# Optimization experiments

Hardware: AMD Instinct MI355X
Metric: run time of the kernel (lower is better)

The kernel has to match this reference:

```python
import jax, jax.numpy as jnp
import numpy as np

EPS = 1e-6


def _mp_match(reps, att, kernel):
    """BiMPM multi-perspective match.
    reps: (B,L,D); att: (B,L,D) or (B,1,D); kernel: (M,D).
    Returns (B,L,1+M): [tanh(sum(reps*att)), tanh(sum_d reps*kernel_m*att)].
    """
    prod = reps * att                                   # (B,L,D)
    cos = jnp.tanh(jnp.sum(prod, axis=-1, keepdims=True))   # (B,L,1)
    mp = jnp.tanh(jnp.einsum('bld,md->blm', prod, kernel))  # (B,L,M)
    return jnp.concatenate([cos, mp], axis=-1)


def setup_inputs() -> dict:
    key = jax.random.key(0)
    ks = jax.random.split(key, 12)
    B, Llt, Lrt, D, M, A = 32, 128, 128, 512, 64, 128
    H = D // 2
    u = lambda k, shape: jax.random.uniform(k, shape, jnp.float32, -0.05, 0.05)  # keras 'uniform' init
    return {
        'reps_lt': jax.random.normal(ks[0], (B, Llt, D), jnp.float32),
        'h_lt_fw': jax.random.normal(ks[1], (B, H), jnp.float32),
        'h_lt_bw': jax.random.normal(ks[2], (B, H), jnp.float32),
        'reps_rt': jax.random.normal(ks[3], (B, Lrt, D), jnp.float32),
        'h_rt_fw': jax.random.normal(ks[4], (B, H), jnp.float32),
        'h_rt_bw': jax.random.normal(ks[5], (B, H), jnp.float32),
        'kernel_full': u(ks[6], (M, D)),
        'kernel_mpool': u(ks[7], (M, D)),
        'attn_w1': u(ks[8], (D, A)),
        'diag_w': u(ks[9], (A,)),
        'kernel_att': u(ks[10], (M, D)),
        'kernel_maxatt': u(ks[11], (M, D)),
    }


def reference(reps_lt, h_lt_fw, h_lt_bw, reps_rt, h_rt_fw, h_rt_bw,
              kernel_full, kernel_mpool, attn_w1, diag_w,
              kernel_att, kernel_maxatt):
    # ---- full match: each left timestep vs last BiLSTM state of right ----
    h_rt = jnp.concatenate([h_rt_fw, h_rt_bw], axis=-1)[:, None, :]  # (B,1,D)
    full = _mp_match(reps_lt, h_rt, kernel_full)                     # (B,Ll,1+M)

    # ---- max-pooling match ----
    # t[b,r,l,m] = tanh(sum_d R[b,r,d]*K[m,d]*L[b,l,d]); max over right positions r
    r_scaled = jnp.einsum('brd,md->brmd', reps_rt, kernel_mpool)     # (B,Lr,M,D)
    t = jnp.tanh(jnp.einsum('brmd,bld->brlm', r_scaled, reps_lt))    # (B,Lr,Ll,M)
    mpool = jnp.max(t, axis=1)                                       # (B,Ll,M)

    # ---- attentive match ----
    a_lt = jnp.tanh(reps_lt @ attn_w1) * diag_w                      # (B,Ll,A)
    a_rt = jnp.tanh(reps_rt @ attn_w1)                               # (B,Lr,A)
    scores = jnp.einsum('bla,bra->blr', a_lt, a_rt)                  # (B,Ll,Lr)
    probs = jax.nn.softmax(scores, axis=-1)
    att = jnp.einsum('blr,brd->bld', probs, reps_rt)                 # (B,Ll,D)
    attentive = _mp_match(reps_lt, att, kernel_att)                  # (B,Ll,1+M)

    # ---- max-attentive match ----
    num = jnp.einsum('bld,brd->blr', reps_lt, reps_rt)
    n_lt = jnp.sqrt(jnp.maximum(jnp.sum(reps_lt * reps_lt, -1), EPS))[:, :, None]
    n_rt = jnp.sqrt(jnp.maximum(jnp.sum(reps_rt * reps_rt, -1), EPS))[:, None, :]
    rel = num / n_rt / n_lt                                          # (B,Ll,Lr)
    idx = jnp.argmax(rel, axis=2)                                    # (B,Ll) int
    max_att = jnp.take_along_axis(reps_rt, idx[:, :, None], axis=1)  # (B,Ll,D)
    maxatt = _mp_match(reps_lt, max_att, kernel_maxatt)              # (B,Ll,1+M)

    return jnp.concatenate([full, mpool, attentive, maxatt], axis=-1)  # (B,Ll,3+4M)
```

## Files before the change

kernel.cpp:

```cpp
#include <hip/hip_runtime.h>
#include <hip/hip_bf16.h>
#include <math.h>
#include <stdint.h>

typedef __attribute__((ext_vector_type(8))) short short8;
typedef __attribute__((ext_vector_type(4))) float float4v;

#define DEV static __device__ __forceinline__

DEV float bflo(unsigned int u) { union { unsigned int i; float f; } v; v.i = u << 16; return v.f; }
DEV float bfhi(unsigned int u) { union { unsigned int i; float f; } v; v.i = u & 0xffff0000u; return v.f; }
DEV unsigned short f2bf(float f) {
    union { float f; unsigned int i; } v; v.f = f;
    unsigned int x = v.i;
    return (unsigned short)((x + 0x7fffu + ((x >> 16) & 1u)) >> 16);
}
DEV unsigned int pack2(float a, float b) { return (unsigned int)f2bf(a) | ((unsigned int)f2bf(b) << 16); }
#if __has_builtin(__builtin_amdgcn_cvt_pk_bf16_f32)
DEV unsigned int pack2_fast(float a, float b) {
    typedef __attribute__((ext_vector_type(2))) short short2v;
    short2v r = __builtin_amdgcn_cvt_pk_bf16_f32(a, b);
    union { short2v s; unsigned int u; } v; v.s = r; return v.u;
}
#else
DEV unsigned int pack2_fast(float a, float b) { return pack2(a, b); }
#endif
DEV void unpack8(uint4 u, float* f) {
    f[0]=bflo(u.x); f[1]=bfhi(u.x); f[2]=bflo(u.y); f[3]=bfhi(u.y);
    f[4]=bflo(u.z); f[5]=bfhi(u.z); f[6]=bflo(u.w); f[7]=bfhi(u.w);
}

DEV void async16(const unsigned short* g, unsigned short* l) {
    __builtin_amdgcn_global_load_lds(
        (const __attribute__((address_space(1))) unsigned int*)g,
        (__attribute__((address_space(3))) unsigned int*)l, 16, 0, 0);
}

__global__ __launch_bounds__(256) void prep_kernel(const float* __restrict__ lt,
                                                   const float* __restrict__ rt,
                                                   const float* __restrict__ kf,
                                                   const float* __restrict__ kmp,
                                                   const float* __restrict__ ka,
                                                   const float* __restrict__ km,
                                                   const float* __restrict__ w1,
                                                   unsigned short* __restrict__ ltb,
                                                   unsigned short* __restrict__ rtb,
                                                   unsigned short* __restrict__ kb,
                                                   unsigned short* __restrict__ w1t,
                                                   unsigned short* __restrict__ rtbT,
                                                   double* __restrict__ rsq) {
    __shared__ double ws2[2][2];
    __shared__ float tile[32][33];
    int bid = blockIdx.x, t = threadIdx.x;
    if (bid < 1024) {
        bool isRt = bid >= 512;
        int base = (isRt ? (bid - 512) : bid) * 8;
        int rl = t >> 7;
        int c  = t & 127;
        const float* srcb = isRt ? rt : lt;
        unsigned short* dstb = isRt ? rtb : ltb;
        #pragma unroll
        for (int p = 0; p < 4; ++p) {
            int row = base + p * 2 + rl;
            const float* src = srcb + (size_t)row * 512;
            float4 v = *(const float4*)(src + c * 4);
            ushort4 o;
            o.x = f2bf(v.x); o.y = f2bf(v.y); o.z = f2bf(v.z); o.w = f2bf(v.w);
            *(ushort4*)(dstb + (size_t)row * 512 + c * 4) = o;
            if (isRt) {
                double s = (double)v.x * v.x + (double)v.y * v.y
                         + (double)v.z * v.z + (double)v.w * v.w;
                #pragma unroll
                for (int off = 1; off < 64; off <<= 1) s += __shfl_xor(s, off, 64);
                if ((c & 63) == 0) ws2[rl][c >> 6] = s;
                __syncthreads();
                if (c == 0) rsq[row] = 1.0 / sqrt(ws2[rl][0] + ws2[rl][1]);
                __syncthreads();
            }
        }
    } else if (bid < 1152) {
        int kbk = bid - 1024;
        int ksel = kbk >> 5;
        const float* src = (ksel == 0) ? kf : (ksel == 1) ? kmp : (ksel == 2) ? ka : km;
        int off = (kbk & 31) * 1024 + t * 4;
        float4 v = *(const float4*)(src + off);
        ushort4 o;
        o.x = f2bf(v.x); o.y = f2bf(v.y); o.z = f2bf(v.z); o.w = f2bf(v.w);
        *(ushort4*)(kb + ksel * 32768 + off) = o;
    } else if (bid < 1216) {
        int b2 = bid - 1152;
        int d0 = (b2 & 15) * 32, a0 = (b2 >> 4) * 32;
        int r = t >> 5, c = t & 31;
        #pragma unroll
        for (int i = 0; i < 32; i += 8)
            tile[r + i][c] = w1[(size_t)(d0 + r + i) * 128 + a0 + c];
        __syncthreads();
        #pragma unroll
        for (int i = 0; i < 32; i += 8)
            w1t[(size_t)(a0 + r + i) * 512 + d0 + c] = f2bf(tile[c][r + i]);
    } else {
        int b3 = bid - 1216;
        int b = b3 >> 6;
        int tid = b3 & 63;
        int d0 = (tid & 15) * 32;
        int r0 = (tid >> 4) * 32;
        int r = t >> 5, c = t & 31;
        #pragma unroll
        for (int i = 0; i < 32; i += 8)
            tile[r + i][c] = rt[(size_t)(b * 128 + r0 + r + i) * 512 + d0 + c];
        __syncthreads();
        #pragma unroll
        for (int i = 0; i < 32; i += 8)
            rtbT[(size_t)(b * 512 + d0 + r + i) * 128 + r0 + c] = f2bf(tile[c][r + i]);
    }
}

__global__ __launch_bounds__(256, 3) void uber_kernel(
        const unsigned short* __restrict__ ltb,
        const unsigned short* __restrict__ rtb,
        const unsigned short* __restrict__ kmb,
        const unsigned short* __restrict__ w1t,
        const float* __restrict__ diag,
        unsigned short* __restrict__ a_all,
        const float* __restrict__ ltf,
        const float* __restrict__ rtf,
        const double* __restrict__ rsq,
        int* __restrict__ idxout,
        float* __restrict__ out) {
    __shared__ __align__(16) unsigned char smem[52224];
    int bx = blockIdx.x;
    int t = threadIdx.x;
    int wave = t >> 6, lane = t & 63;
    int q = lane >> 4, col = lane & 15, kq = q * 8;

    if (bx < 2048) {
        int xcd = bx & 7, jj = bx >> 3;
        int b = xcd * 4 + (jj >> 6);
        int m = jj & 63;
        unsigned short* ltS = (unsigned short*)smem;
        unsigned short* rtL = (unsigned short*)(smem + 16384);
        float (*mx)[2] = (float(*)[2])(smem + 16384 + 32768);
        int wl = wave & 1, wr = wave >> 1;
        const unsigned short* ltp = ltb + (size_t)b * 65536;
        const unsigned short* rtp = rtb + (size_t)b * 65536;
        const unsigned short* kr = kmb + (size_t)m * 512;
        int srow = t >> 3, cg8 = t & 7, cg = cg8 * 8;
        int gsw = (cg8 ^ (srow & 7)) * 8;
        int wbase = (t & ~63) * 8;

        #pragma unroll
        for (int it = 0; it < 4; ++it)
            async16(rtp + (size_t)(it * 32 + srow) * 512 + gsw,
                    rtL + it * 2048 + wbase);
        uint4 pk = *(const uint4*)(kr + cg);
        uint4 plt[4];
        #pragma unroll
        for (int it = 0; it < 4; ++it)
            plt[it] = *(const uint4*)(ltp + (size_t)(it * 32 + srow) * 512 + cg);

        float4v acc[4][4] = {};
        for (int k0i = 0; k0i < 8; ++k0i) {
            float kf8[8]; unpack8(pk, kf8);
            #pragma unroll
            for (int it = 0; it < 4; ++it) {
                int row = it * 32 + srow;
                float lf[8]; unpack8(plt[it], lf);
                uint4 s;
                s.x = pack2_fast(lf[0] * kf8[0], lf[1] * kf8[1]);
                s.y = pack2_fast(lf[2] * kf8[2], lf[3] * kf8[3]);
                s.z = pack2_fast(lf[4] * kf8[4], lf[5] * kf8[5]);
                s.w = pack2_fast(lf[6] * kf8[6], lf[7] * kf8[7]);
                *(uint4*)&ltS[row * 64 + gsw] = s;
            }
            __syncthreads();
            if (k0i < 7) {
                int k0n = (k0i + 1) * 64;
                int bofs = ((k0i + 1) & 1) * 8192;
                #pragma unroll
                for (int it = 0; it < 4; ++it)
                    async16(rtp + (size_t)(it * 32 + srow) * 512 + k0n + gsw,
                            rtL + bofs + it * 2048 + wbase);
                pk = *(const uint4*)(kr + k0n + cg);
                #pragma unroll
                for (int it = 0; it < 4; ++it)
                    plt[it] = *(const uint4*)(ltp + (size_t)(it * 32 + srow) * 512 + k0n + cg);
            }
            const unsigned short* rb = rtL + (k0i & 1) * 8192;
            #pragma unroll
            for (int kk = 0; kk < 64; kk += 32) {
                short8 af[4], bfr[4];
                #pragma unroll
                for (int i = 0; i < 4; ++i) {
                    int rowA = wl * 64 + i * 16 + col;
                    int slotA = ((kk >> 3) + q) ^ (rowA & 7);
                    af[i] = *(const short8*)&ltS[rowA * 64 + slotA * 8];
                }
                #pragma unroll
                for (int j = 0; j < 4; ++j) {
                    int row = wr * 64 + j * 16 + col;
                    int slot = ((kk >> 3) + q) ^ (row & 7);
                    bfr[j] = *(const short8*)&rb[row * 64 + slot * 8];
                }
                #pragma unroll
                for (int i = 0; i < 4; ++i)
                    #pragma unroll
                    for (int j = 0; j < 4; ++j)
                        acc[i][j] = __builtin_amdgcn_mfma_f32_16x16x32_bf16(af[i], bfr[j], acc[i][j], 0, 0, 0);
            }
            __syncthreads();
        }
        #pragma unroll
        for (int i = 0; i < 4; ++i)
            #pragma unroll
            for (int ii = 0; ii < 4; ++ii) {
                float v = fmaxf(fmaxf(acc[i][0][ii], acc[i][1][ii]), fmaxf(acc[i][2][ii], acc[i][3][ii]));
                #pragma unroll
                for (int off = 1; off < 16; off <<= 1) v = fmaxf(v, __shfl_xor(v, off, 64));
                if (col == 0) mx[wl * 64 + i * 16 + q * 4 + ii][wr] = v;
            }
        __syncthreads();
        if (t < 128)
            out[((size_t)(b * 128 + t)) * 259 + 65 + m] = tanhf(fmaxf(mx[t][0], mx[t][1]));

    } else if (bx < 2560) {
        int idA = bx - 2048;
        int xcd = idA & 7, jj = idA >> 3;
        int b = xcd * 4 + (jj >> 4);
        int L0 = (jj & 15) * 8;
        float* ltS = (float*)smem;
        float* buf = (float*)(smem + 16384);
        double* dvs = (double*)(smem + 49152);
        float* wv1 = (float*)(smem + 49152 + 128);
        float* wv2 = wv1 + 16;
        int* wi1 = (int*)(wv2 + 16);
        int* wi2 = wi1 + 16;
        int* candi = wi2 + 16;
        {
            int row = t >> 5, c0 = (t & 31) * 16;
            const float* src = ltf + ((size_t)(b * 128 + L0 + row)) * 512 + c0;
            #pragma unroll
            for (int i = 0; i < 4; ++i)
                *(float4*)&ltS[row * 512 + c0 + i * 4] = *(const float4*)(src + i * 4);
        }
        int lg = t >> 7;
        int rg = (t >> 2) & 31;
        int ds = t & 3;
        float acc[4][4] = {{0.f}};
        for (int p = 0; p < 8; ++p) {
            __syncthreads();
            {
                int row = t >> 1, c0 = (t & 1) * 32;
                const float* src = rtf + ((size_t)(b * 128 + row)) * 512 + p * 64 + c0;
                float f[32];
                #pragma unroll
                for (int i = 0; i < 8; ++i)
                    *(float4*)&f[i * 4] = *(const float4*)(src + i * 4);
                int base = row * 64;
                #pragma unroll
                for (int gg = 0; gg < 4; ++gg) {
                    int g = (t & 1) * 4 + gg;
                    int o = ((g ^ (row & 7)) * 8);
                    #pragma unroll
                    for (int k = 0; k < 8; ++k) buf[base + o + k] = f[gg * 8 + k];
                }
            }
            __syncthreads();
            #pragma unroll
            for (int sub = 0; sub < 2; ++sub) {
                int dloc = ds * 16 + sub * 8;
                int dglob = p * 64 + dloc;
                float a[4][8];
                #pragma unroll
                for (int i = 0; i < 4; ++i)
                    #pragma unroll
                    for (int k = 0; k < 8; ++k) a[i][k] = ltS[(lg * 4 + i) * 512 + dglob + k];
                int g = dloc >> 3;
                #pragma unroll
                for (int j = 0; j < 4; ++j) {
                    int r = rg + j * 32;
                    const float* rp = &buf[r * 64 + ((g ^ (r & 7)) * 8)];
                    float rv[8];
                    #pragma unroll
                    for (int k = 0; k < 8; ++k) rv[k] = rp[k];
                    #pragma unroll
                    for (int i = 0; i < 4; ++i)
                        #pragma unroll
                        for (int k = 0; k < 8; ++k)
                            acc[i][j] = fmaf(a[i][k], rv[k], acc[i][j]);
                }
            }
        }
        #pragma unroll
        for (int i = 0; i < 4; ++i)
            #pragma unroll
            for (int j = 0; j < 4; ++j) {
                acc[i][j] += __shfl_xor(acc[i][j], 1, 64);
                acc[i][j] += __shfl_xor(acc[i][j], 2, 64);
            }
        float v1[4], v2[4]; int i1[4], i2[4];
        #pragma unroll
        for (int i = 0; i < 4; ++i) {
            v1[i] = -3.0e38f; v2[i] = -3.0e38f; i1[i] = 0; i2[i] = 1;
            #pragma unroll
            for (int j = 0; j < 4; ++j) {
                int r = rg + j * 32;
                float s = acc[i][j] * (float)rsq[b * 128 + r];
                if (s > v1[i]) { v2[i] = v1[i]; i2[i] = i1[i]; v1[i] = s; i1[i] = r; }
                else if (s > v2[i]) { v2[i] = s; i2[i] = r; }
            }
        }
        #pragma unroll
        for (int off = 4; off < 64; off <<= 1) {
            #pragma unroll
            for (int i = 0; i < 4; ++i) {
                float u1 = __shfl_xor(v1[i], off, 64); int j1 = __shfl_xor(i1[i], off, 64);
                float u2 = __shfl_xor(v2[i], off, 64); int j2 = __shfl_xor(i2[i], off, 64);
                if (u1 > v1[i]) {
                    float ov = v1[i]; int oi = i1[i];
                    v1[i] = u1; i1[i] = j1;
                    if (u2 > ov) { v2[i] = u2; i2[i] = j2; } else { v2[i] = ov; i2[i] = oi; }
                } else if (u1 > v2[i]) { v2[i] = u1; i2[i] = j1; }
            }
        }
        if (lane == 0) {
            #pragma unroll
            for (int i = 0; i < 4; ++i) {
                int l = lg * 4 + i, h = wave & 1;
                wv1[l * 2 + h] = v1[i]; wi1[l * 2 + h] = i1[i];
                wv2[l * 2 + h] = v2[i]; wi2[l * 2 + h] = i2[i];
            }
        }
        __syncthreads();
        if (t < 8) {
            float a1 = wv1[t * 2], a2 = wv2[t * 2]; int ai1 = wi1[t * 2], ai2 = wi2[t * 2];
            float b1 = wv1[t * 2 + 1], b2 = wv2[t * 2 + 1]; int bi1 = wi1[t * 2 + 1], bi2 = wi2[t * 2 + 1];
            int ri1, ri2;
            if (b1 > a1) {
                ri1 = bi1;
                if (b2 > a1) { ri2 = bi2; } else { ri2 = ai1; }
            } else {
                ri1 = ai1;
                if (b1 > a2) { ri2 = bi1; } else { ri2 = ai2; }
            }
            candi[t * 2] = ri1; candi[t * 2 + 1] = ri2;
            (void)a2; (void)b2; (void)ai2; (void)bi2;
        }
        __syncthreads();
        {
            int dotid = t >> 4;
            int sub = t & 15;
            int l = dotid >> 1, c = dotid & 1;
            int r = candi[l * 2 + c];
            const float* lrow = ltf + ((size_t)(b * 128 + L0 + l)) * 512;
            const float* rrow = rtf + ((size_t)(b * 128 + r)) * 512;
            double s = 0.0;
            #pragma unroll 8
            for (int k = 0; k < 32; ++k) {
                int d = sub * 32 + k;
                s = fma((double)lrow[d], (double)rrow[d], s);
            }
            #pragma unroll
            for (int off = 1; off < 16; off <<= 1) s += __shfl_xor(s, off, 64);
            if (sub == 0) dvs[l * 2 + c] = s * rsq[b * 128 + r];
        }
        __syncthreads();
        if (t < 8) {
            int ia = candi[t * 2], ib = candi[t * 2 + 1];
            double va = dvs[t * 2], vb = dvs[t * 2 + 1];
            int res = (vb > va || (vb == va && ib < ia)) ? ib : ia;
            idxout[b * 128 + L0 + t] = res;
        }

    } else {
        int R0 = (bx - 2560) * 32;
        unsigned short (*aS)[72] = (unsigned short(*)[72])smem;
        unsigned short (*bS)[72] = (unsigned short(*)[72])(smem + 4608);
        float* diagS = (float*)(smem + 4608 + 18432);
        int wl = wave & 1, wr = wave >> 1;
        if (t < 128) diagS[t] = diag[t];
        const unsigned short* src = (R0 < 4096) ? (ltb + (size_t)R0 * 512) : (rtb + (size_t)(R0 - 4096) * 512);
        float4v acc[4] = {};
        for (int k0 = 0; k0 < 512; k0 += 64) {
            {
                int row = t >> 3, cg = (t & 7) * 8;
                *(uint4*)&aS[row][cg] = *(const uint4*)(src + (size_t)row * 512 + k0 + cg);
            }
            #pragma unroll
            for (int it = 0; it < 4; ++it) {
                int id = it * 256 + t;
                int row = id >> 3, cg = (id & 7) * 8;
                *(uint4*)&bS[row][cg] = *(const uint4*)(w1t + (size_t)row * 512 + k0 + cg);
            }
            __syncthreads();
            #pragma unroll
            for (int kk = 0; kk < 64; kk += 32) {
                short8 af = *(const short8*)&aS[wl * 16 + col][kk + kq];
                #pragma unroll
                for (int j = 0; j < 4; ++j) {
                    short8 bf = *(const short8*)&bS[wr * 64 + j * 16 + col][kk + kq];
                    acc[j] = __builtin_amdgcn_mfma_f32_16x16x32_bf16(af, bf, acc[j], 0, 0, 0);
                }
            }
            __syncthreads();
        }
        bool isLt = (R0 < 4096);
        #pragma unroll
        for (int j = 0; j < 4; ++j)
            #pragma unroll
            for (int ii = 0; ii < 4; ++ii) {
                int rowl = wl * 16 + q * 4 + ii;
                int n = wr * 64 + j * 16 + col;
                float v = tanhf(acc[j][ii]);
                if (isLt) v *= diagS[n];
                a_all[((size_t)(R0 + rowl)) * 128 + n] = f2bf(v);
            }
    }
}

__global__ __launch_bounds__(512, 4) void tail_kernel(
        const unsigned short* __restrict__ a_all,
        const unsigned short* __restrict__ rtb,
        const unsigned short* __restrict__ rtbT,
        const float* __restrict__ ltf,
        const unsigned short* __restrict__ kb,
        const float* __restrict__ hfw,
        const float* __restrict__ hbw,
        const int* __restrict__ idxp,
        float* __restrict__ out) {
    __shared__ __align__(16) unsigned char smem[81664];
    int bx = blockIdx.x;
    int t = threadIdx.x;
    int wave = t >> 6, lane = t & 63;
    int q = lane >> 4, col = lane & 15, kq = q * 8;

    if (bx < 256) {
        int b = bx & 31, lg = bx >> 5;
        int L0 = lg * 16;
        unsigned short (*altS)[136]  = (unsigned short(*)[136])(smem);
        unsigned short (*artS)[136]  = (unsigned short(*)[136])(smem + 4352);
        unsigned short (*prodsF)[520]= (unsigned short(*)[520])(smem + 55552);
        float (*pmax)[8] = (float(*)[8])(smem + 80640);
        float (*psum)[8] = (float(*)[8])(smem + 81152);
        const unsigned short* kb_att = kb + 2 * 32768;

        if (t < 256) {
            int row = t >> 4, c0 = (t & 15) * 8;
            *(uint4*)&altS[row][c0] = *(const uint4*)(a_all + ((size_t)(b * 128 + L0 + row)) * 128 + c0);
        }
        {
            int row = t >> 2, c0 = (t & 3) * 32;
            const unsigned short* src = a_all + ((size_t)(4096 + b * 128 + row)) * 128 + c0;
            #pragma unroll
            for (int i = 0; i < 4; ++i)
                *(uint4*)&artS[row][c0 + i * 8] = *(const uint4*)(src + i * 8);
        }
        __syncthreads();

        float4v acc = {};
        #pragma unroll
        for (int kk = 0; kk < 128; kk += 32) {
            short8 af = *(const short8*)&altS[col][kk + kq];
            short8 bf = *(const short8*)&artS[wave * 16 + col][kk + kq];
            acc = __builtin_amdgcn_mfma_f32_16x16x32_bf16(af, bf, acc, 0, 0, 0);
        }
        float m4[4], p4[4];
        #pragma unroll
        for (int ii = 0; ii < 4; ++ii) {
            float v = acc[ii];
            #pragma unroll
            for (int off = 1; off < 16; off <<= 1) v = fmaxf(v, __shfl_xor(v, off, 64));
            m4[ii] = v;
        }
        if (col == 0) {
            #pragma unroll
            for (int ii = 0; ii < 4; ++ii) pmax[q * 4 + ii][wave] = m4[ii];
        }
        __syncthreads();
        #pragma unroll
        for (int ii = 0; ii < 4; ++ii) {
            float M = pmax[q * 4 + ii][0];
            #pragma unroll
            for (int w = 1; w < 8; ++w) M = fmaxf(M, pmax[q * 4 + ii][w]);
            p4[ii] = expf(acc[ii] - M);
            float s = p4[ii];
            #pragma unroll
            for (int off = 1; off < 16; off <<= 1) s += __shfl_xor(s, off, 64);
            m4[ii] = s;
        }
        if (col == 0) {
            #pragma unroll
            for (int ii = 0; ii < 4; ++ii) psum[q * 4 + ii][wave] = m4[ii];
        }
        __syncthreads();
        unsigned short* Pb = (unsigned short*)smem;
        #pragma unroll
        for (int ii = 0; ii < 4; ++ii) {
            float S = psum[q * 4 + ii][0] + psum[q * 4 + ii][1] + psum[q * 4 + ii][2] + psum[q * 4 + ii][3]
                    + psum[q * 4 + ii][4] + psum[q * 4 + ii][5] + psum[q * 4 + ii][6] + psum[q * 4 + ii][7];
            Pb[(q * 4 + ii) * 136 + wave * 16 + col] = f2bf(p4[ii] / S);
        }

        unsigned short* Bc = (unsigned short*)(smem + 4352);
        float* attF = (float*)(smem + 39168);
        const unsigned short* rtT = rtbT + (size_t)b * 65536;
        for (int cc = 0; cc < 4; ++cc) {
            #pragma unroll
            for (int i = 0; i < 4; ++i) {
                int rid = i * 32 + (t >> 4);
                int d   = (rid >> 4) * 64 + cc * 16 + (rid & 15);
                int sg  = (t & 15) ^ (rid & 15);
                async16(rtT + (size_t)d * 128 + sg * 8, Bc + i * 4096 + t * 8);
            }
            __syncthreads();
            float4v pacc = {};
            #pragma unroll
            for (int ks = 0; ks < 4; ++ks) {
                short8 afP = *(const short8*)&Pb[col * 136 + ks * 32 + kq];
                short8 bfB = *(const short8*)&Bc[(wave * 16 + col) * 128 + (((ks * 4 + q) ^ col) * 8)];
                pacc = __builtin_amdgcn_mfma_f32_16x16x32_bf16(afP, bfB, pacc, 0, 0, 0);
            }
            #pragma unroll
            for (int ii = 0; ii < 4; ++ii)
                attF[(q * 4 + ii) * 512 + wave * 64 + cc * 16 + col] = pacc[ii];
            __syncthreads();
        }

        int l = t >> 5, cd = t & 31;
        float a8[2][8];
        #pragma unroll
        for (int pass = 0; pass < 2; ++pass) {
            *(float4*)&a8[pass][0] = *(const float4*)&attF[l * 512 + pass * 256 + cd * 8];
            *(float4*)&a8[pass][4] = *(const float4*)&attF[l * 512 + pass * 256 + cd * 8 + 4];
        }
        __syncthreads();

        int grow = b * 128 + L0 + l;
        const float* ltrow = ltf + (size_t)grow * 512;
        float csum = 0.f;
        #pragma unroll
        for (int pass = 0; pass < 2; ++pass) {
            int d0 = pass * 256 + cd * 8;
            float lf[8];
            *(float4*)&lf[0] = *(const float4*)(ltrow + d0);
            *(float4*)&lf[4] = *(const float4*)(ltrow + d0 + 4);
            float pf[8];
            #pragma unroll
            for (int k = 0; k < 8; ++k) { pf[k] = lf[k] * a8[pass][k]; csum += pf[k]; }
            uint4 o;
            o.x = pack2(pf[0], pf[1]); o.y = pack2(pf[2], pf[3]);
            o.z = pack2(pf[4], pf[5]); o.w = pack2(pf[6], pf[7]);
            *(uint4*)&prodsF[l][d0] = o;
        }
        #pragma unroll
        for (int off = 1; off < 32; off <<= 1) csum += __shfl_xor(csum, off, 64);
        if (cd == 0) out[(size_t)grow * 259 + 129] = tanhf(csum);

        unsigned short* Ks = &artS[0][0];
        float* red = (float*)(smem + 39168);
        for (int half = 0; half < 2; ++half) {
            __syncthreads();
            {
                int row = t >> 4, c0 = (t & 15) * 32;
                const unsigned short* src = kb_att + ((size_t)(half * 32 + row)) * 512 + c0;
                #pragma unroll
                for (int i = 0; i < 4; ++i)
                    *(uint4*)&Ks[row * 520 + c0 + i * 8] = *(const uint4*)(src + i * 8);
            }
            __syncthreads();
            float4v pacc[2] = {};
            #pragma unroll
            for (int kk = 0; kk < 64; kk += 32) {
                short8 af = *(const short8*)&prodsF[col][wave * 64 + kk + kq];
                #pragma unroll
                for (int j = 0; j < 2; ++j) {
                    short8 bf = *(const short8*)&Ks[(j * 16 + col) * 520 + wave * 64 + kk + kq];
                    pacc[j] = __builtin_amdgcn_mfma_f32_16x16x32_bf16(af, bf, pacc[j], 0, 0, 0);
                }
            }
            #pragma unroll
            for (int j = 0; j < 2; ++j)
                #pragma unroll
                for (int ii = 0; ii < 4; ++ii)
                    red[((wave * 2 + j) * 16 + q * 4 + ii) * 16 + col] = pacc[j][ii];
            __syncthreads();
            {
                int ll = t >> 5, jm = t & 31;
                int j = jm >> 4, mc = jm & 15;
                float s = 0.f;
                #pragma unroll
                for (int w = 0; w < 8; ++w) s += red[((w * 2 + j) * 16 + ll) * 16 + mc];
                out[((size_t)(b * 128 + L0 + ll)) * 259 + 130 + half * 32 + jm] = tanhf(s);
            }
        }

    } else {
        int idB = bx - 256;
        int lg = idB & 7, b = (idB >> 3) & 31;
        int mode = (idB >> 8) ? 2 : 0;
        int L0 = lg * 16;
        unsigned short (*prods)[520] = (unsigned short(*)[520])smem;
        unsigned short* Ks = (unsigned short*)(smem + 16640);
        float* red = (float*)(smem + 49920);
        const unsigned short* Kp = kb + (size_t)((mode == 0) ? 0 : 3 * 32768);
        int obase = (mode == 0) ? 0 : 194;

        if (t < 256) {
            int l = t >> 4, c = t & 15;
            int grow = b * 128 + L0 + l;
            const float* ltrow = ltf + (size_t)grow * 512;
            const unsigned short* avrow = 0;
            if (mode == 2) avrow = rtb + ((size_t)(b * 128 + idxp[grow])) * 512;
            float csum = 0.f;
            #pragma unroll
            for (int pass = 0; pass < 4; ++pass) {
                int d0 = pass * 128 + c * 8;
                float lf[8], af[8], pf[8];
                *(float4*)&lf[0] = *(const float4*)(ltrow + d0);
                *(float4*)&lf[4] = *(const float4*)(ltrow + d0 + 4);
                if (mode == 0) {
                    const float* h = (d0 < 256) ? (hfw + b * 256 + d0) : (hbw + b * 256 + d0 - 256);
                    *(float4*)&af[0] = *(const float4*)h;
                    *(float4*)&af[4] = *(const float4*)(h + 4);
                } else {
                    uint4 av = *(const uint4*)(avrow + d0);
                    unpack8(av, af);
                }
                #pragma unroll
                for (int k = 0; k < 8; ++k) { pf[k] = lf[k] * af[k]; csum += pf[k]; }
                uint4 o;
                o.x = pack2(pf[0], pf[1]); o.y = pack2(pf[2], pf[3]);
                o.z = pack2(pf[4], pf[5]); o.w = pack2(pf[6], pf[7]);
                *(uint4*)&prods[l][d0] = o;
            }
            #pragma unroll
            for (int off = 1; off < 16; off <<= 1) csum += __shfl_xor(csum, off, 64);
            if (c == 0) out[(size_t)grow * 259 + obase] = tanhf(csum);
        }
        for (int half = 0; half < 2; ++half) {
            {
                int row = t >> 4, c0 = (t & 15) * 32;
                const unsigned short* src = Kp + ((size_t)(half * 32 + row)) * 512 + c0;
                #pragma unroll
                for (int i = 0; i < 4; ++i)
                    *(uint4*)&Ks[row * 520 + c0 + i * 8] = *(const uint4*)(src + i * 8);
            }
            __syncthreads();
            float4v acc2[2] = {};
            #pragma unroll
            for (int kk = 0; kk < 64; kk += 32) {
                short8 af = *(const short8*)&prods[col][wave * 64 + kk + kq];
                #pragma unroll
                for (int j = 0; j < 2; ++j) {
                    short8 bf = *(const short8*)&Ks[(j * 16 + col) * 520 + wave * 64 + kk + kq];
                    acc2[j] = __builtin_amdgcn_mfma_f32_16x16x32_bf16(af, bf, acc2[j], 0, 0, 0);
                }
            }
            #pragma unroll
            for (int j = 0; j < 2; ++j)
                #pragma unroll
                for (int ii = 0; ii < 4; ++ii)
                    red[((wave * 2 + j) * 16 + q * 4 + ii) * 16 + col] = acc2[j][ii];
            __syncthreads();
            {
                int ll = t >> 5, jm = t & 31;
                int j = jm >> 4, mc = jm & 15;
                float s = 0.f;
                #pragma unroll
                for (int w = 0; w < 8; ++w) s += red[((w * 2 + j) * 16 + ll) * 16 + mc];
                out[((size_t)(b * 128 + L0 + ll)) * 259 + obase + 1 + half * 32 + jm] = tanhf(s);
            }
            __syncthreads();
        }
    }
}

extern "C" void kernel_launch(void* const* d_in, const int* in_sizes, int n_in,
                              void* d_out, int out_size, void* d_ws, size_t ws_size,
                              hipStream_t stream) {
    const float* lt  = (const float*)d_in[0];
    const float* rt  = (const float*)d_in[3];
    const float* hfw = (const float*)d_in[4];
    const float* hbw = (const float*)d_in[5];
    const float* kf  = (const float*)d_in[6];
    const float* kmp = (const float*)d_in[7];
    const float* w1  = (const float*)d_in[8];
    const float* dia = (const float*)d_in[9];
    const float* ka  = (const float*)d_in[10];
    const float* km  = (const float*)d_in[11];
    float* out = (float*)d_out;

    char* wsb = (char*)d_ws;
    unsigned short* ltb16 = (unsigned short*)(wsb);
    unsigned short* rtb16 = (unsigned short*)(wsb + 4194304);
    unsigned short* kb16  = (unsigned short*)(wsb + 8388608);
    unsigned short* w1t   = (unsigned short*)(wsb + 8650752);
    unsigned short* a_all = (unsigned short*)(wsb + 8781824);
    unsigned short* rtbT  = (unsigned short*)(wsb + 10878976);
    double*         rsq   = (double*)(wsb + 15073280);
    int*            idx   = (int*)(wsb + 15106048);

    prep_kernel<<<3264, 256, 0, stream>>>(lt, rt, kf, kmp, ka, km, w1, ltb16, rtb16, kb16, w1t, rtbT, rsq);
    uber_kernel<<<2816, 256, 0, stream>>>(ltb16, rtb16, kb16 + 32768, w1t, dia, a_all,
                                          lt, rt, rsq, idx, out);
    tail_kernel<<<768, 512, 0, stream>>>(a_all, rtb16, rtbT, lt, kb16, hfw, hbw, idx, out);
}
```

Baseline: 174.4 us.

## Move max-pooling GEMM blocks into tail kernel, interleaved with attentive/match blocks

Moves the max-pooling match blocks out of the middle kernel into the final kernel. They now run as 512-thread blocks with 8 waves, each wave holding a narrower 4x2 accumulator tile. Blocks are interleaved in groups of 11 (8 mpool, 1 attentive, 2 mp-match), so the independent mpool work can overlap with the dependent attentive and max-attentive work. The middle kernel shrinks to the argmax and attention-projection blocks. The trade-off is fewer accumulators per wave and a heavier last kernel.

```diff
diff --git a/kernel.cpp b/kernel.cpp
--- a/kernel.cpp
+++ b/kernel.cpp
@@ -115,115 +115,24 @@
     }
 }
 
-__global__ __launch_bounds__(256, 3) void uber_kernel(
+__global__ __launch_bounds__(256, 3) void mid_kernel(
         const unsigned short* __restrict__ ltb,
         const unsigned short* __restrict__ rtb,
-        const unsigned short* __restrict__ kmb,
         const unsigned short* __restrict__ w1t,
         const float* __restrict__ diag,
         unsigned short* __restrict__ a_all,
         const float* __restrict__ ltf,
         const float* __restrict__ rtf,
         const double* __restrict__ rsq,
-        int* __restrict__ idxout,
-        float* __restrict__ out) {
+        int* __restrict__ idxout) {
     __shared__ __align__(16) unsigned char smem[52224];
     int bx = blockIdx.x;
     int t = threadIdx.x;
     int wave = t >> 6, lane = t & 63;
     int q = lane >> 4, col = lane & 15, kq = q * 8;
 
-    if (bx < 2048) {
-        int xcd = bx & 7, jj = bx >> 3;
-        int b = xcd * 4 + (jj >> 6);
-        int m = jj & 63;
-        unsigned short* ltS = (unsigned short*)smem;
-        unsigned short* rtL = (unsigned short*)(smem + 16384);
-        float (*mx)[2] = (float(*)[2])(smem + 16384 + 32768);
-        int wl = wave & 1, wr = wave >> 1;
-        const unsigned short* ltp = ltb + (size_t)b * 65536;
-        const unsigned short* rtp = rtb + (size_t)b * 65536;
-        const unsigned short* kr = kmb + (size_t)m * 512;
-        int srow = t >> 3, cg8 = t & 7, cg = cg8 * 8;
-        int gsw = (cg8 ^ (srow & 7)) * 8;
-        int wbase = (t & ~63) * 8;
-
-        #pragma unroll
-        for (int it = 0; it < 4; ++it)
-            async16(rtp + (size_t)(it * 32 + srow) * 512 + gsw,
-                    rtL + it * 2048 + wbase);
-        uint4 pk = *(const uint4*)(kr + cg);
-        uint4 plt[4];
-        #pragma unroll
-        for (int it = 0; it < 4; ++it)
-            plt[it] = *(const uint4*)(ltp + (size_t)(it * 32 + srow) * 512 + cg);
-
-        float4v acc[4][4] = {};
-        for (int k0i = 0; k0i < 8; ++k0i) {
-            float kf8[8]; unpack8(pk, kf8);
-            #pragma unroll
-            for (int it = 0; it < 4; ++it) {
-                int row = it * 32 + srow;
-                float lf[8]; unpack8(plt[it], lf);
-                uint4 s;
-                s.x = pack2_fast(lf[0] * kf8[0], lf[1] * kf8[1]);
-                s.y = pack2_fast(lf[2] * kf8[2], lf[3] * kf8[3]);
-                s.z = pack2_fast(lf[4] * kf8[4], lf[5] * kf8[5]);
-                s.w = pack2_fast(lf[6] * kf8[6], lf[7] * kf8[7]);
-                *(uint4*)&ltS[row * 64 + gsw] = s;
-            }
-            __syncthreads();
-            if (k0i < 7) {
-                int k0n = (k0i + 1) * 64;
-                int bofs = ((k0i + 1) & 1) * 8192;
-                #pragma unroll
-                for (int it = 0; it < 4; ++it)
-                    async16(rtp + (size_t)(it * 32 + srow) * 512 + k0n + gsw,
-                            rtL + bofs + it * 2048 + wbase);
-                pk = *(const uint4*)(kr + k0n + cg);
-                #pragma unroll
-                for (int it = 0; it < 4; ++it)
-                    plt[it] = *(const uint4*)(ltp + (size_t)(it * 32 + srow) * 512 + k0n + cg);
-            }
-            const unsigned short* rb = rtL + (k0i & 1) * 8192;
-            #pragma unroll
-            for (int kk = 0; kk < 64; kk += 32) {
-                short8 af[4], bfr[4];
-                #pragma unroll
-                for (int i = 0; i < 4; ++i) {
-                    int rowA = wl * 64 + i * 16 + col;
-                    int slotA = ((kk >> 3) + q) ^ (rowA & 7);
-                    af[i] = *(const short8*)&ltS[rowA * 64 + slotA * 8];
-                }
-                #pragma unroll
-                for (int j = 0; j < 4; ++j) {
-                    int row = wr * 64 + j * 16 + col;
-                    int slot = ((kk >> 3) + q) ^ (row & 7);
-                    bfr[j] = *(const short8*)&rb[row * 64 + slot * 8];
-                }
-                #pragma unroll
-                for (int i = 0; i < 4; ++i)
-                    #pragma unroll
-                    for (int j = 0; j < 4; ++j)
-                        acc[i][j] = __builtin_amdgcn_mfma_f32_16x16x32_bf16(af[i], bfr[j], acc[i][j], 0, 0, 0);
-            }
-            __syncthreads();
-        }
-        #pragma unroll
-        for (int i = 0; i < 4; ++i)
-            #pragma unroll
-            for (int ii = 0; ii < 4; ++ii) {
-                float v = fmaxf(fmaxf(acc[i][0][ii], acc[i][1][ii]), fmaxf(acc[i][2][ii], acc[i][3][ii]));
-                #pragma unroll
-                for (int off = 1; off < 16; off <<= 1) v = fmaxf(v, __shfl_xor(v, off, 64));
-                if (col == 0) mx[wl * 64 + i * 16 + q * 4 + ii][wr] = v;
-            }
-        __syncthreads();
-        if (t < 128)
-            out[((size_t)(b * 128 + t)) * 259 + 65 + m] = tanhf(fmaxf(mx[t][0], mx[t][1]));
-
-    } else if (bx < 2560) {
-        int idA = bx - 2048;
+    if (bx < 512) {
+        int idA = bx;
         int xcd = idA & 7, jj = idA >> 3;
         int b = xcd * 4 + (jj >> 4);
         int L0 = (jj & 15) * 8;
@@ -372,7 +281,7 @@
         }
 
     } else {
-        int R0 = (bx - 2560) * 32;
+        int R0 = (bx - 512) * 32;
         unsigned short (*aS)[72] = (unsigned short(*)[72])smem;
         unsigned short (*bS)[72] = (unsigned short(*)[72])(smem + 4608);
         float* diagS = (float*)(smem + 4608 + 18432);
@@ -417,9 +326,11 @@
     }
 }
 
-__global__ __launch_bounds__(512, 4) void tail_kernel(
+__global__ __launch_bounds__(512, 4) void main_kernel(
+        const unsigned short* __restrict__ ltb,
+        const unsigned short* __restrict__ rtb,
+        const unsigned short* __restrict__ kmb,
         const unsigned short* __restrict__ a_all,
-        const unsigned short* __restrict__ rtb,
         const unsigned short* __restrict__ rtbT,
         const float* __restrict__ ltf,
         const unsigned short* __restrict__ kb,
@@ -433,8 +344,103 @@
     int wave = t >> 6, lane = t & 63;
     int q = lane >> 4, col = lane & 15, kq = q * 8;
 
-    if (bx < 256) {
-        int b = bx & 31, lg = bx >> 5;
+    int bxg = bx / 11;
+    int r11 = bx - bxg * 11;
+
+    if (r11 < 8) {
+        int mp = bxg * 8 + r11;
+        int xcd = mp & 7, jj = mp >> 3;
+        int b = xcd * 4 + (jj >> 6);
+        int m = jj & 63;
+        unsigned short* ltS = (unsigned short*)smem;
+        unsigned short* rtL = (unsigned short*)(smem + 16384);
+        float (*mx)[4] = (float(*)[4])(smem + 49152);
+        int wl = wave & 1, wr = wave >> 1;
+        const unsigned short* ltp = ltb + (size_t)b * 65536;
+        const unsigned short* rtp = rtb + (size_t)b * 65536;
+        const unsigned short* kr = kmb + (size_t)m * 512;
+        int srow = t >> 3, cg8 = t & 7, cg = cg8 * 8;
+        int gsw = (cg8 ^ (srow & 7)) * 8;
+
+        #pragma unroll
+        for (int it = 0; it < 2; ++it)
+            async16(rtp + (size_t)(it * 64 + srow) * 512 + gsw,
+                    rtL + it * 4096 + t * 8);
+        uint4 pk = *(const uint4*)(kr + cg);
+        uint4 plt[2];
+        #pragma unroll
+        for (int it = 0; it < 2; ++it)
+            plt[it] = *(const uint4*)(ltp + (size_t)(it * 64 + srow) * 512 + cg);
+
+        float4v acc[4][2] = {};
+        for (int k0i = 0; k0i < 8; ++k0i) {
+            float kf8[8]; unpack8(pk, kf8);
+            #pragma unroll
+            for (int it = 0; it < 2; ++it) {
+                int row = it * 64 + srow;
+                float lf[8]; unpack8(plt[it], lf);
+                uint4 s;
+                s.x = pack2_fast(lf[0] * kf8[0], lf[1] * kf8[1]);
+                s.y = pack2_fast(lf[2] * kf8[2], lf[3] * kf8[3]);
+                s.z = pack2_fast(lf[4] * kf8[4], lf[5] * kf8[5]);
+                s.w = pack2_fast(lf[6] * kf8[6], lf[7] * kf8[7]);
+                *(uint4*)&ltS[row * 64 + gsw] = s;
+            }
+            __syncthreads();
+            if (k0i < 7) {
+                int k0n = (k0i + 1) * 64;
+                int bofs = ((k0i + 1) & 1) * 8192;
+                #pragma unroll
+                for (int it = 0; it < 2; ++it)
+                    async16(rtp + (size_t)(it * 64 + srow) * 512 + k0n + gsw,
+                            rtL + bofs + it * 4096 + t * 8);
+                pk = *(const uint4*)(kr + k0n + cg);
+                #pragma unroll
+                for (int it = 0; it < 2; ++it)
+                    plt[it] = *(const uint4*)(ltp + (size_t)(it * 64 + srow) * 512 + k0n + cg);
+            }
+            const unsigned short* rb = rtL + (k0i & 1) * 8192;
+            #pragma unroll
+            for (int kk = 0; kk < 64; kk += 32) {
+                short8 af[4], bfr[2];
+                #pragma unroll
+                for (int i = 0; i < 4; ++i) {
+                    int rowA = wl * 64 + i * 16 + col;
+                    int slotA = ((kk >> 3) + q) ^ (rowA & 7);
+                    af[i] = *(const short8*)&ltS[rowA * 64 + slotA * 8];
+                }
+                #pragma unroll
+                for (int j = 0; j < 2; ++j) {
+                    int row = wr * 32 + j * 16 + col;
+                    int slot = ((kk >> 3) + q) ^ (row & 7);
+                    bfr[j] = *(const short8*)&rb[row * 64 + slot * 8];
+                }
+                #pragma unroll
+                for (int i = 0; i < 4; ++i)
+                    #pragma unroll
+                    for (int j = 0; j < 2; ++j)
+                        acc[i][j] = __builtin_amdgcn_mfma_f32_16x16x32_bf16(af[i], bfr[j], acc[i][j], 0, 0, 0);
+            }
+            __syncthreads();
+        }
+        #pragma unroll
+        for (int i = 0; i < 4; ++i)
+            #pragma unroll
+            for (int ii = 0; ii < 4; ++ii) {
+                float v = fmaxf(acc[i][0][ii], acc[i][1][ii]);
+                #pragma unroll
+                for (int off = 1; off < 16; off <<= 1) v = fmaxf(v, __shfl_xor(v, off, 64));
+                if (col == 0) mx[wl * 64 + i * 16 + q * 4 + ii][wr] = v;
+            }
+        __syncthreads();
+        if (t < 128) {
+            float v = fmaxf(fmaxf(mx[t][0], mx[t][1]), fmaxf(mx[t][2], mx[t][3]));
+            out[((size_t)(b * 128 + t)) * 259 + 65 + m] = tanhf(v);
+        }
+
+    } else if (r11 == 8) {
+        int id = bxg;
+        int b = id & 31, lg = id >> 5;
         int L0 = lg * 16;
         unsigned short (*altS)[136]  = (unsigned short(*)[136])(smem);
         unsigned short (*artS)[136]  = (unsigned short(*)[136])(smem + 4352);
@@ -594,7 +600,7 @@
         }
 
     } else {
-        int idB = bx - 256;
+        int idB = bxg * 2 + (r11 - 9);
         int lg = idB & 7, b = (idB >> 3) & 31;
         int mode = (idB >> 8) ? 2 : 0;
         int L0 = lg * 16;
@@ -700,7 +706,7 @@
     int*            idx   = (int*)(wsb + 15106048);
 
     prep_kernel<<<3264, 256, 0, stream>>>(lt, rt, kf, kmp, ka, km, w1, ltb16, rtb16, kb16, w1t, rtbT, rsq);
-    uber_kernel<<<2816, 256, 0, stream>>>(ltb16, rtb16, kb16 + 32768, w1t, dia, a_all,
-                                          lt, rt, rsq, idx, out);
-    tail_kernel<<<768, 512, 0, stream>>>(a_all, rtb16, rtbT, lt, kb16, hfw, hbw, idx, out);
+    mid_kernel<<<768, 256, 0, stream>>>(ltb16, rtb16, w1t, dia, a_all, lt, rt, rsq, idx);
+    main_kernel<<<2816, 512, 0, stream>>>(ltb16, rtb16, kb16 + 32768, a_all, rtbT,
+                                          lt, kb16, hfw, hbw, idx, out);
 }
```

Measured after the change: 192.6 us. 10.4% more time.

## Compute max-attentive similarity with bf16 MFMA and defer fp64 refinement to tail kernel

Applied to the files above, without the earlier changes.

The max-attentive cosine-similarity matmul used to run in fp32 scalar FMAs across 512 blocks. It now runs as a bf16 MFMA GEMM in 32 blocks, one per batch, each producing a 128x128 tile. Each wave keeps top-2 candidates per left row, so every row gets 4 packed candidate indices. The fp64 re-scoring of those candidates and the argmax selection move into the tail kernel's mode-2 blocks, which removes the separate idx pass from the uber kernel. This relies on bf16 top-2 per half always containing the true argmax. It also puts 32 large GEMM blocks on the critical path and adds fp64 dot products to the tail kernel.

```diff
diff --git a/kernel.cpp b/kernel.cpp
--- a/kernel.cpp
+++ b/kernel.cpp
@@ -122,10 +122,8 @@
         const unsigned short* __restrict__ w1t,
         const float* __restrict__ diag,
         unsigned short* __restrict__ a_all,
-        const float* __restrict__ ltf,
-        const float* __restrict__ rtf,
         const double* __restrict__ rsq,
-        int* __restrict__ idxout,
+        unsigned int* __restrict__ candp,
         float* __restrict__ out) {
     __shared__ __align__(16) unsigned char smem[52224];
     int bx = blockIdx.x;
@@ -222,157 +220,109 @@
         if (t < 128)
             out[((size_t)(b * 128 + t)) * 259 + 65 + m] = tanhf(fmaxf(mx[t][0], mx[t][1]));
 
-    } else if (bx < 2560) {
-        int idA = bx - 2048;
-        int xcd = idA & 7, jj = idA >> 3;
-        int b = xcd * 4 + (jj >> 4);
-        int L0 = (jj & 15) * 8;
-        float* ltS = (float*)smem;
-        float* buf = (float*)(smem + 16384);
-        double* dvs = (double*)(smem + 49152);
-        float* wv1 = (float*)(smem + 49152 + 128);
-        float* wv2 = wv1 + 16;
-        int* wi1 = (int*)(wv2 + 16);
-        int* wi2 = wi1 + 16;
-        int* candi = wi2 + 16;
-        {
-            int row = t >> 5, c0 = (t & 31) * 16;
-            const float* src = ltf + ((size_t)(b * 128 + L0 + row)) * 512 + c0;
-            #pragma unroll
-            for (int i = 0; i < 4; ++i)
-                *(float4*)&ltS[row * 512 + c0 + i * 4] = *(const float4*)(src + i * 4);
-        }
-        int lg = t >> 7;
-        int rg = (t >> 2) & 31;
-        int ds = t & 3;
-        float acc[4][4] = {{0.f}};
-        for (int p = 0; p < 8; ++p) {
-            __syncthreads();
-            {
-                int row = t >> 1, c0 = (t & 1) * 32;
-                const float* src = rtf + ((size_t)(b * 128 + row)) * 512 + p * 64 + c0;
-                float f[32];
-                #pragma unroll
-                for (int i = 0; i < 8; ++i)
-                    *(float4*)&f[i * 4] = *(const float4*)(src + i * 4);
-                int base = row * 64;
-                #pragma unroll
-                for (int gg = 0; gg < 4; ++gg) {
-                    int g = (t & 1) * 4 + gg;
-                    int o = ((g ^ (row & 7)) * 8);
-                    #pragma unroll
-                    for (int k = 0; k < 8; ++k) buf[base + o + k] = f[gg * 8 + k];
-                }
-            }
-            __syncthreads();
-            #pragma unroll
-            for (int sub = 0; sub < 2; ++sub) {
-                int dloc = ds * 16 + sub * 8;
-                int dglob = p * 64 + dloc;
-                float a[4][8];
+    } else if (bx < 2080) {
+        int sb = bx - 2048;
+        int xcd = sb & 7;
+        int b = xcd * 4 + (sb >> 3);
+        unsigned short* ltS = (unsigned short*)smem;
+        unsigned short* rtL = (unsigned short*)(smem + 16384);
+        float* rsqf = (float*)(smem + 49152);
+        unsigned int (*candL)[2] = (unsigned int(*)[2])(smem + 49664);
+        int wl = wave & 1, wr = wave >> 1;
+        const unsigned short* ltp = ltb + (size_t)b * 65536;
+        const unsigned short* rtp = rtb + (size_t)b * 65536;
+        int srow = t >> 3, cg8 = t & 7, cg = cg8 * 8;
+        int gsw = (cg8 ^ (srow & 7)) * 8;
+        int wbase = (t & ~63) * 8;
+
+        #pragma unroll
+        for (int it = 0; it < 4; ++it)
+            async16(rtp + (size_t)(it * 32 + srow) * 512 + gsw,
+                    rtL + it * 2048 + wbase);
+        uint4 plt[4];
+        #pragma unroll
+        for (int it = 0; it < 4; ++it)
+            plt[it] = *(const uint4*)(ltp + (size_t)(it * 32 + srow) * 512 + cg);
+        if (t < 128) rsqf[t] = (float)rsq[b * 128 + t];
+
+        float4v acc[4][4] = {};
+        for (int k0i = 0; k0i < 8; ++k0i) {
+            #pragma unroll
+            for (int it = 0; it < 4; ++it) {
+                int row = it * 32 + srow;
+                *(uint4*)&ltS[row * 64 + gsw] = plt[it];
+            }
+            __syncthreads();
+            if (k0i < 7) {
+                int k0n = (k0i + 1) * 64;
+                int bofs = ((k0i + 1) & 1) * 8192;
+                #pragma unroll
+                for (int it = 0; it < 4; ++it)
+                    async16(rtp + (size_t)(it * 32 + srow) * 512 + k0n + gsw,
+                            rtL + bofs + it * 2048 + wbase);
+                #pragma unroll
+                for (int it = 0; it < 4; ++it)
+                    plt[it] = *(const uint4*)(ltp + (size_t)(it * 32 + srow) * 512 + k0n + cg);
+            }
+            const unsigned short* rb = rtL + (k0i & 1) * 8192;
+            #pragma unroll
+            for (int kk = 0; kk < 64; kk += 32) {
+                short8 af[4], bfr[4];
+                #pragma unroll
+                for (int i = 0; i < 4; ++i) {
+                    int rowA = wl * 64 + i * 16 + col;
+                    int slotA = ((kk >> 3) + q) ^ (rowA & 7);
+                    af[i] = *(const short8*)&ltS[rowA * 64 + slotA * 8];
+                }
+                #pragma unroll
+                for (int j = 0; j < 4; ++j) {
+                    int row = wr * 64 + j * 16 + col;
+                    int slot = ((kk >> 3) + q) ^ (row & 7);
+                    bfr[j] = *(const short8*)&rb[row * 64 + slot * 8];
+                }
                 #pragma unroll
                 for (int i = 0; i < 4; ++i)
                     #pragma unroll
-                    for (int k = 0; k < 8; ++k) a[i][k] = ltS[(lg * 4 + i) * 512 + dglob + k];
-                int g = dloc >> 3;
+                    for (int j = 0; j < 4; ++j)
+                        acc[i][j] = __builtin_amdgcn_mfma_f32_16x16x32_bf16(af[i], bfr[j], acc[i][j], 0, 0, 0);
+            }
+            __syncthreads();
+        }
+        float rq[4];
+        #pragma unroll
+        for (int j = 0; j < 4; ++j) rq[j] = rsqf[wr * 64 + j * 16 + col];
+        #pragma unroll
+        for (int i = 0; i < 4; ++i)
+            #pragma unroll
+            for (int ii = 0; ii < 4; ++ii) {
+                float v1 = -3.0e38f, v2 = -3.0e38f; int i1 = 0, i2 = 1;
                 #pragma unroll
                 for (int j = 0; j < 4; ++j) {
-                    int r = rg + j * 32;
-                    const float* rp = &buf[r * 64 + ((g ^ (r & 7)) * 8)];
-                    float rv[8];
-                    #pragma unroll
-                    for (int k = 0; k < 8; ++k) rv[k] = rp[k];
-                    #pragma unroll
-                    for (int i = 0; i < 4; ++i)
-                        #pragma unroll
-                        for (int k = 0; k < 8; ++k)
-                            acc[i][j] = fmaf(a[i][k], rv[k], acc[i][j]);
-                }
-            }
-        }
-        #pragma unroll
-        for (int i = 0; i < 4; ++i)
-            #pragma unroll
-            for (int j = 0; j < 4; ++j) {
-                acc[i][j] += __shfl_xor(acc[i][j], 1, 64);
-                acc[i][j] += __shfl_xor(acc[i][j], 2, 64);
-            }
-        float v1[4], v2[4]; int i1[4], i2[4];
-        #pragma unroll
-        for (int i = 0; i < 4; ++i) {
-            v1[i] = -3.0e38f; v2[i] = -3.0e38f; i1[i] = 0; i2[i] = 1;
-            #pragma unroll
-            for (int j = 0; j < 4; ++j) {
-                int r = rg + j * 32;
-                float s = acc[i][j] * (float)rsq[b * 128 + r];
-                if (s > v1[i]) { v2[i] = v1[i]; i2[i] = i1[i]; v1[i] = s; i1[i] = r; }
-                else if (s > v2[i]) { v2[i] = s; i2[i] = r; }
-            }
-        }
-        #pragma unroll
-        for (int off = 4; off < 64; off <<= 1) {
-            #pragma unroll
-            for (int i = 0; i < 4; ++i) {
-                float u1 = __shfl_xor(v1[i], off, 64); int j1 = __shfl_xor(i1[i], off, 64);
-                float u2 = __shfl_xor(v2[i], off, 64); int j2 = __shfl_xor(i2[i], off, 64);
-                if (u1 > v1[i]) {
-                    float ov = v1[i]; int oi = i1[i];
-                    v1[i] = u1; i1[i] = j1;
-                    if (u2 > ov) { v2[i] = u2; i2[i] = j2; } else { v2[i] = ov; i2[i] = oi; }
-                } else if (u1 > v2[i]) { v2[i] = u1; i2[i] = j1; }
-            }
-        }
-        if (lane == 0) {
-            #pragma unroll
-            for (int i = 0; i < 4; ++i) {
-                int l = lg * 4 + i, h = wave & 1;
-                wv1[l * 2 + h] = v1[i]; wi1[l * 2 + h] = i1[i];
-                wv2[l * 2 + h] = v2[i]; wi2[l * 2 + h] = i2[i];
-            }
-        }
-        __syncthreads();
-        if (t < 8) {
-            float a1 = wv1[t * 2], a2 = wv2[t * 2]; int ai1 = wi1[t * 2], ai2 = wi2[t * 2];
-            float b1 = wv1[t * 2 + 1], b2 = wv2[t * 2 + 1]; int bi1 = wi1[t * 2 + 1], bi2 = wi2[t * 2 + 1];
-            int ri1, ri2;
-            if (b1 > a1) {
-                ri1 = bi1;
-                if (b2 > a1) { ri2 = bi2; } else { ri2 = ai1; }
-            } else {
-                ri1 = ai1;
-                if (b1 > a2) { ri2 = bi1; } else { ri2 = ai2; }
-            }
-            candi[t * 2] = ri1; candi[t * 2 + 1] = ri2;
-            (void)a2; (void)b2; (void)ai2; (void)bi2;
-        }
-        __syncthreads();
-        {
-            int dotid = t >> 4;
-            int sub = t & 15;
-            int l = dotid >> 1, c = dotid & 1;
-            int r = candi[l * 2 + c];
-            const float* lrow = ltf + ((size_t)(b * 128 + L0 + l)) * 512;
-            const float* rrow = rtf + ((size_t)(b * 128 + r)) * 512;
-            double s = 0.0;
-            #pragma unroll 8
-            for (int k = 0; k < 32; ++k) {
-                int d = sub * 32 + k;
-                s = fma((double)lrow[d], (double)rrow[d], s);
-            }
-            #pragma unroll
-            for (int off = 1; off < 16; off <<= 1) s += __shfl_xor(s, off, 64);
-            if (sub == 0) dvs[l * 2 + c] = s * rsq[b * 128 + r];
-        }
-        __syncthreads();
-        if (t < 8) {
-            int ia = candi[t * 2], ib = candi[t * 2 + 1];
-            double va = dvs[t * 2], vb = dvs[t * 2 + 1];
-            int res = (vb > va || (vb == va && ib < ia)) ? ib : ia;
-            idxout[b * 128 + L0 + t] = res;
-        }
+                    int rc = wr * 64 + j * 16 + col;
+                    float s = acc[i][j][ii] * rq[j];
+                    if (s > v1) { v2 = v1; i2 = i1; v1 = s; i1 = rc; }
+                    else if (s > v2) { v2 = s; i2 = rc; }
+                }
+                #pragma unroll
+                for (int off = 1; off < 16; off <<= 1) {
+                    float u1 = __shfl_xor(v1, off, 64); int j1 = __shfl_xor(i1, off, 64);
+                    float u2 = __shfl_xor(v2, off, 64); int j2 = __shfl_xor(i2, off, 64);
+                    if (u1 > v1) {
+                        float ov = v1; int oi = i1;
+                        v1 = u1; i1 = j1;
+                        if (u2 > ov) { v2 = u2; i2 = j2; } else { v2 = ov; i2 = oi; }
+                    } else if (u1 > v2) { v2 = u1; i2 = j1; }
+                }
+                if (col == 0)
+                    candL[wl * 64 + i * 16 + q * 4 + ii][wr] =
+                        (unsigned int)i1 | ((unsigned int)i2 << 8);
+            }
+        __syncthreads();
+        if (t < 128)
+            candp[b * 128 + t] = candL[t][0] | (candL[t][1] << 16);
 
     } else {
-        int R0 = (bx - 2560) * 32;
+        int R0 = (bx - 2080) * 32;
         unsigned short (*aS)[72] = (unsigned short(*)[72])smem;
         unsigned short (*bS)[72] = (unsigned short(*)[72])(smem + 4608);
         float* diagS = (float*)(smem + 4608 + 18432);
@@ -422,10 +372,12 @@
         const unsigned short* __restrict__ rtb,
         const unsigned short* __restrict__ rtbT,
         const float* __restrict__ ltf,
+        const float* __restrict__ rtf,
+        const double* __restrict__ rsq,
         const unsigned short* __restrict__ kb,
         const float* __restrict__ hfw,
         const float* __restrict__ hbw,
-        const int* __restrict__ idxp,
+        const unsigned int* __restrict__ candp,
         float* __restrict__ out) {
     __shared__ __align__(16) unsigned char smem[81664];
     int bx = blockIdx.x;
@@ -601,15 +553,48 @@
         unsigned short (*prods)[520] = (unsigned short(*)[520])smem;
         unsigned short* Ks = (unsigned short*)(smem + 16640);
         float* red = (float*)(smem + 49920);
+        double* dvs2 = (double*)(smem + 66304);
+        int* idxl = (int*)(smem + 66816);
         const unsigned short* Kp = kb + (size_t)((mode == 0) ? 0 : 3 * 32768);
         int obase = (mode == 0) ? 0 : 194;
+
+        if (mode == 2) {
+            int dotid = t >> 3, sub = t & 7;
+            int l = dotid >> 2, c = dotid & 3;
+            unsigned int cpl = candp[b * 128 + L0 + l];
+            int r = (cpl >> (c * 8)) & 0xff;
+            const float* lrow = ltf + ((size_t)(b * 128 + L0 + l)) * 512;
+            const float* rrow = rtf + ((size_t)(b * 128 + r)) * 512;
+            double s = 0.0;
+            #pragma unroll 8
+            for (int k = 0; k < 64; ++k) {
+                int d = sub * 64 + k;
+                s = fma((double)lrow[d], (double)rrow[d], s);
+            }
+            #pragma unroll
+            for (int off = 1; off < 8; off <<= 1) s += __shfl_xor(s, off, 64);
+            if (sub == 0) dvs2[dotid] = s * rsq[b * 128 + r];
+            __syncthreads();
+            if (t < 16) {
+                unsigned int cl = candp[b * 128 + L0 + t];
+                int bi = 256; double bv = -1.0e300;
+                #pragma unroll
+                for (int cc = 0; cc < 4; ++cc) {
+                    int rr = (cl >> (cc * 8)) & 0xff;
+                    double v = dvs2[t * 4 + cc];
+                    if (v > bv || (v == bv && rr < bi)) { bv = v; bi = rr; }
+                }
+                idxl[t] = bi;
+            }
+            __syncthreads();
+        }
 
         if (t < 256) {
             int l = t >> 4, c = t & 15;
             int grow = b * 128 + L0 + l;
             const float* ltrow = ltf + (size_t)grow * 512;
             const unsigned short* avrow = 0;
-            if (mode == 2) avrow = rtb + ((size_t)(b * 128 + idxp[grow])) * 512;
+            if (mode == 2) avrow = rtb + ((size_t)(b * 128 + idxl[l])) * 512;
             float csum = 0.f;
             #pragma unroll
             for (int pass = 0; pass < 4; ++pass) {
@@ -697,10 +682,10 @@
     unsigned short* a_all = (unsigned short*)(wsb + 8781824);
     unsigned short* rtbT  = (unsigned short*)(wsb + 10878976);
     double*         rsq   = (double*)(wsb + 15073280);
-    int*            idx   = (int*)(wsb + 15106048);
+    unsigned int*   candp = (unsigned int*)(wsb + 15106048);
 
     prep_kernel<<<3264, 256, 0, stream>>>(lt, rt, kf, kmp, ka, km, w1, ltb16, rtb16, kb16, w1t, rtbT, rsq);
-    uber_kernel<<<2816, 256, 0, stream>>>(ltb16, rtb16, kb16 + 32768, w1t, dia, a_all,
-                                          lt, rt, rsq, idx, out);
-    tail_kernel<<<768, 512, 0, stream>>>(a_all, rtb16, rtbT, lt, kb16, hfw, hbw, idx, out);
-}
+    uber_kernel<<<2336, 256, 0, stream>>>(ltb16, rtb16, kb16 + 32768, w1t, dia, a_all,
+                                          rsq, candp, out);
+    tail_kernel<<<768, 512, 0, stream>>>(a_all, rtb16, rtbT, lt, rt, rsq, kb16, hfw, hbw, candp, out);
+}
```

Result: no change. 176.9 us (+1.4%).
